# Kernel tuning notes

Hardware: AMD Instinct MI355X
Metric: run time of the kernel (lower is better)

Reference implementation:

```python
import jax, jax.numpy as jnp
import numpy as np

B, S, L = 4, 4096, 256

def _dense_init(key, fan_in, fan_out):
    lim = float(np.sqrt(6.0 / (fan_in + fan_out)))  # glorot_uniform (keras Dense default)
    return jax.random.uniform(key, (fan_in, fan_out), minval=-lim, maxval=lim, dtype=jnp.float32)

def setup_inputs() -> dict:
    key = jax.random.key(0)
    ks = jax.random.split(key, 12)
    causal = jnp.triu(jnp.ones((S, S), jnp.float32), k=1)  # 1 where future -> masked
    return {
        "tar_position": jax.random.uniform(ks[0], (B, S), dtype=jnp.float32),
        "current_pos": jax.random.uniform(ks[1], (B, S), dtype=jnp.float32),
        "tar_inp": jax.random.normal(ks[2], (B, S), dtype=jnp.float32),
        "training": 0,
        "pos_mask": jnp.zeros((B, S, S), jnp.float32),  # unused in call
        "tar_mask": jnp.broadcast_to(causal, (B, S, S)),
        "wq_w": _dense_init(ks[3], 2, L), "wq_b": jnp.zeros((L,), jnp.float32),
        "wk_w": _dense_init(ks[4], 2, L), "wk_b": jnp.zeros((L,), jnp.float32),
        "wv_w": _dense_init(ks[5], 1, L), "wv_b": jnp.zeros((L,), jnp.float32),
        "a2_w": _dense_init(ks[6], L, 128), "a2_b": jnp.zeros((128,), jnp.float32),
        "a3_w": _dense_init(ks[7], 1, 128), "a3_b": jnp.zeros((128,), jnp.float32),
        "a4_w": _dense_init(ks[8], 128, 32), "a4_b": jnp.zeros((32,), jnp.float32),
        "a5_w": _dense_init(ks[9], 32, 2), "a5_b": jnp.zeros((2,), jnp.float32),
    }

def reference(tar_position, current_pos, tar_inp, training, pos_mask, tar_mask,
              wq_w, wq_b, wk_w, wk_b, wv_w, wv_b,
              a2_w, a2_b, a3_w, a3_b, a4_w, a4_b, a5_w, a5_b):
    cp = current_pos[:, :, None]                         # [B,S,1]
    tar = jnp.stack([tar_position, tar_inp], axis=-1)    # [B,S,2]
    # matmul([B,S,l,1],[B,S,1,1]) == elementwise scale by current_pos
    q = (tar @ wq_w + wq_b) * cp                         # [B,S,L]
    k = (tar @ wk_w + wk_b) * cp                         # [B,S,L]
    v = tar_inp[:, :, None] * wv_w[0] + wv_b             # [B,S,L] (Dense fan_in=1)
    scale = 1.0 / jnp.sqrt(jnp.asarray(q.shape[-1], q.dtype))
    scores = jnp.einsum('bsl,btl->bst', q, k) * scale + tar_mask * (-1e9)
    attn = jax.nn.softmax(scores, axis=-1)               # [B,S,S]
    tar_attn = jnp.einsum('bst,btl->bsl', attn, v)       # [B,S,L]
    h = tar_attn @ a2_w + a2_b + cp * a3_w[0] + a3_b     # [B,S,128]
    h = jax.nn.leaky_relu(h, 0.2)                        # tf.nn.leaky_relu alpha=0.2
    h = jax.nn.leaky_relu(h @ a4_w + a4_b, 0.2)          # [B,S,32]
    out = h @ a5_w + a5_b                                # [B,S,2]
    return jnp.squeeze(out)
```

## Files before the change

### kernel.cpp

```cpp
#include <hip/hip_runtime.h>


#define SEQ 4096
#define NB 4


__global__ __launch_bounds__(256) void pre_kernel(
    const float* __restrict__ wq_w, const float* __restrict__ wq_b,
    const float* __restrict__ wk_w, const float* __restrict__ wk_b,
    const float* __restrict__ wv_w, const float* __restrict__ wv_b,
    const float* __restrict__ a2_w, const float* __restrict__ a2_b,
    const float* __restrict__ a3_w, const float* __restrict__ a3_b,
    float* __restrict__ ws)
{
    int tid = threadIdx.x;
    if (tid < 128) {
        float c1 = 0.f, c3 = 0.f;
        for (int l = 0; l < 256; ++l) {
            float a2 = a2_w[l * 128 + tid];
            c1 += wv_w[l] * a2;
            c3 += wv_b[l] * a2;
        }
        ws[16 + tid]  = c1;
        ws[160 + tid] = a3_w[tid];
        ws[288 + tid] = c3 + a2_b[tid] + a3_b[tid];
    } else if (tid < 128 + 9) {
        int idx = tid - 128;
        int i = idx / 3, j = idx % 3;
        const float* qv = (i == 0) ? wq_w : (i == 1) ? (wq_w + 256) : wq_b;
        const float* kv = (j == 0) ? wk_w : (j == 1) ? (wk_w + 256) : wk_b;
        float m = 0.f;
        for (int l = 0; l < 256; ++l) m += qv[l] * kv[l];
        ws[i * 3 + j] = m;
    }
}

__global__ __launch_bounds__(256) void attn_kernel(
    const float* __restrict__ tp,
    const float* __restrict__ cp,
    const float* __restrict__ ti,
    const float* __restrict__ ws,
    float* __restrict__ A)
{
    const int wave = (blockIdx.x * blockDim.x + threadIdx.x) >> 6;
    const int lane = threadIdx.x & 63;
    const int b = wave >> 11;
    const int r = wave & 2047;

    const float M00 = ws[0], M01 = ws[1], M02 = ws[2];
    const float M10 = ws[3], M11 = ws[4], M12 = ws[5];
    const float M20 = ws[6], M21 = ws[7], M22 = ws[8];
    const float scale = 0.0625f;

    const float* __restrict__ tpb = tp + b * SEQ;
    const float* __restrict__ cpb = cp + b * SEQ;
    const float* __restrict__ tib = ti + b * SEQ;

    #pragma unroll
    for (int pick = 0; pick < 2; ++pick) {
        const int s = pick ? (SEQ - 1 - r) : r;
        const float cps = cpb[s], tps = tpb[s], tis = tib[s];
        const float x0 = cps * tps, x1 = cps * tis, x2 = cps;
        const float d0 = scale * (M00 * x0 + M10 * x1 + M20 * x2);
        const float d1 = scale * (M01 * x0 + M11 * x1 + M21 * x2);
        const float d2 = scale * (M02 * x0 + M12 * x1 + M22 * x2);

        float lsum = 0.f, asum = 0.f;
        for (int t = lane; t <= s; t += 64) {
            const float cpt = cpb[t];
            const float tpt = tpb[t];
            const float tit = tib[t];
            const float sc = cpt * (d0 * tpt + d1 * tit + d2);
            const float w = __expf(sc);
            lsum += w;
            asum += w * tit;
        }
        #pragma unroll
        for (int off = 32; off; off >>= 1) {
            lsum += __shfl_down(lsum, off, 64);
            asum += __shfl_down(asum, off, 64);
        }
        if (lane == 0) A[b * SEQ + s] = asum / lsum;
    }
}

__global__ __launch_bounds__(64) void mlp_kernel(
    const float* __restrict__ A,
    const float* __restrict__ cp,
    const float* __restrict__ ws,
    const float* __restrict__ a4_w,
    const float* __restrict__ a4_b,
    const float* __restrict__ a5_w,
    const float* __restrict__ a5_b,
    float* __restrict__ out)
{
    __shared__ float sc1[128], sc2[128], sc3[128];
    __shared__ float sa4[128 * 32];
    const int tid = threadIdx.x;
    for (int i = tid; i < 128; i += 64) {
        sc1[i] = ws[16 + i];
        sc2[i] = ws[160 + i];
        sc3[i] = ws[288 + i];
    }
    for (int i = tid; i < 128 * 32; i += 64) sa4[i] = a4_w[i];
    __syncthreads();

    const int p = blockIdx.x * 64 + tid;
    const float Av = A[p], cpv = cp[p];

    float acc[32];
    #pragma unroll
    for (int j2 = 0; j2 < 32; ++j2) acc[j2] = a4_b[j2];

    for (int j = 0; j < 128; ++j) {
        float h = Av * sc1[j] + cpv * sc2[j] + sc3[j];
        h = (h >= 0.f) ? h : 0.2f * h;
        #pragma unroll
        for (int j2 = 0; j2 < 32; ++j2) acc[j2] += h * sa4[j * 32 + j2];
    }

    float o0 = a5_b[0], o1 = a5_b[1];
    #pragma unroll
    for (int j2 = 0; j2 < 32; ++j2) {
        const float h2 = (acc[j2] >= 0.f) ? acc[j2] : 0.2f * acc[j2];
        o0 += h2 * a5_w[j2 * 2 + 0];
        o1 += h2 * a5_w[j2 * 2 + 1];
    }
    out[p * 2 + 0] = o0;
    out[p * 2 + 1] = o1;
}

extern "C" void kernel_launch(void* const* d_in, const int* in_sizes, int n_in,
                              void* d_out, int out_size, void* d_ws, size_t ws_size,
                              hipStream_t stream) {
    const float* tp   = (const float*)d_in[0];
    const float* cp   = (const float*)d_in[1];
    const float* ti   = (const float*)d_in[2];
    const float* wq_w = (const float*)d_in[6];
    const float* wq_b = (const float*)d_in[7];
    const float* wk_w = (const float*)d_in[8];
    const float* wk_b = (const float*)d_in[9];
    const float* wv_w = (const float*)d_in[10];
    const float* wv_b = (const float*)d_in[11];
    const float* a2_w = (const float*)d_in[12];
    const float* a2_b = (const float*)d_in[13];
    const float* a3_w = (const float*)d_in[14];
    const float* a3_b = (const float*)d_in[15];
    const float* a4_w = (const float*)d_in[16];
    const float* a4_b = (const float*)d_in[17];
    const float* a5_w = (const float*)d_in[18];
    const float* a5_b = (const float*)d_in[19];

    float* ws  = (float*)d_ws;
    float* A   = ws + 512;
    float* out = (float*)d_out;

    hipLaunchKernelGGL(pre_kernel, dim3(1), dim3(256), 0, stream,
                       wq_w, wq_b, wk_w, wk_b, wv_w, wv_b,
                       a2_w, a2_b, a3_w, a3_b, ws);
    hipLaunchKernelGGL(attn_kernel, dim3(2048), dim3(256), 0, stream,
                       tp, cp, ti, ws, A);
    hipLaunchKernelGGL(mlp_kernel, dim3(256), dim3(64), 0, stream,
                       A, cp, ws, a4_w, a4_b, a5_w, a5_b, out);
}
```

Before: 475.2 us.

## Pack per-position features into float4 array and unroll attention loop by two

```diff
diff --git a/kernel.cpp b/kernel.cpp
--- a/kernel.cpp
+++ b/kernel.cpp
@@ -6,6 +6,8 @@
 
 
 __global__ __launch_bounds__(256) void pre_kernel(
+    const float* __restrict__ tp, const float* __restrict__ cp,
+    const float* __restrict__ ti,
     const float* __restrict__ wq_w, const float* __restrict__ wq_b,
     const float* __restrict__ wk_w, const float* __restrict__ wk_b,
     const float* __restrict__ wv_w, const float* __restrict__ wv_b,
@@ -13,32 +15,35 @@
     const float* __restrict__ a3_w, const float* __restrict__ a3_b,
     float* __restrict__ ws)
 {
-    int tid = threadIdx.x;
+    const int tid = threadIdx.x;
+    const int p = blockIdx.x * 256 + tid;
+    const float cpv = cp[p], tpv = tp[p], tiv = ti[p];
+    float4* X = (float4*)(ws + 1024);
+    X[p] = make_float4(cpv * tpv, cpv * tiv, cpv, tiv);
+
+    if (blockIdx.x != 0) return;
     if (tid < 128) {
         float c1 = 0.f, c3 = 0.f;
         for (int l = 0; l < 256; ++l) {
-            float a2 = a2_w[l * 128 + tid];
-            c1 += wv_w[l] * a2;
-            c3 += wv_b[l] * a2;
+            const float a2 = a2_w[l * 128 + tid];
+            c1 = fmaf(wv_w[l], a2, c1);
+            c3 = fmaf(wv_b[l], a2, c3);
         }
         ws[16 + tid]  = c1;
         ws[160 + tid] = a3_w[tid];
         ws[288 + tid] = c3 + a2_b[tid] + a3_b[tid];
-    } else if (tid < 128 + 9) {
-        int idx = tid - 128;
-        int i = idx / 3, j = idx % 3;
+    } else if (tid < 137) {
+        const int idx = tid - 128;
+        const int i = idx / 3, j = idx % 3;
         const float* qv = (i == 0) ? wq_w : (i == 1) ? (wq_w + 256) : wq_b;
         const float* kv = (j == 0) ? wk_w : (j == 1) ? (wk_w + 256) : wk_b;
         float m = 0.f;
-        for (int l = 0; l < 256; ++l) m += qv[l] * kv[l];
-        ws[i * 3 + j] = m;
+        for (int l = 0; l < 256; ++l) m = fmaf(qv[l], kv[l], m);
+        ws[i * 3 + j] = m * 0.0625f;
     }
 }
 
 __global__ __launch_bounds__(256) void attn_kernel(
-    const float* __restrict__ tp,
-    const float* __restrict__ cp,
-    const float* __restrict__ ti,
     const float* __restrict__ ws,
     float* __restrict__ A)
 {
@@ -50,30 +55,35 @@
     const float M00 = ws[0], M01 = ws[1], M02 = ws[2];
     const float M10 = ws[3], M11 = ws[4], M12 = ws[5];
     const float M20 = ws[6], M21 = ws[7], M22 = ws[8];
-    const float scale = 0.0625f;
 
-    const float* __restrict__ tpb = tp + b * SEQ;
-    const float* __restrict__ cpb = cp + b * SEQ;
-    const float* __restrict__ tib = ti + b * SEQ;
+    const float4* __restrict__ Xb = (const float4*)(ws + 1024) + b * SEQ;
 
     #pragma unroll
     for (int pick = 0; pick < 2; ++pick) {
         const int s = pick ? (SEQ - 1 - r) : r;
-        const float cps = cpb[s], tps = tpb[s], tis = tib[s];
-        const float x0 = cps * tps, x1 = cps * tis, x2 = cps;
-        const float d0 = scale * (M00 * x0 + M10 * x1 + M20 * x2);
-        const float d1 = scale * (M01 * x0 + M11 * x1 + M21 * x2);
-        const float d2 = scale * (M02 * x0 + M12 * x1 + M22 * x2);
+        const float4 xs = Xb[s];
+        const float d0 = M00 * xs.x + M10 * xs.y + M20 * xs.z;
+        const float d1 = M01 * xs.x + M11 * xs.y + M21 * xs.z;
+        const float d2 = M02 * xs.x + M12 * xs.y + M22 * xs.z;
 
         float lsum = 0.f, asum = 0.f;
-        for (int t = lane; t <= s; t += 64) {
-            const float cpt = cpb[t];
-            const float tpt = tpb[t];
-            const float tit = tib[t];
-            const float sc = cpt * (d0 * tpt + d1 * tit + d2);
-            const float w = __expf(sc);
-            lsum += w;
-            asum += w * tit;
+        int t = lane;
+        for (; t + 64 <= s; t += 128) {
+            const float4 xa = Xb[t];
+            const float4 xb = Xb[t + 64];
+            const float sa = fmaf(d0, xa.x, fmaf(d1, xa.y, d2 * xa.z));
+            const float sb = fmaf(d0, xb.x, fmaf(d1, xb.y, d2 * xb.z));
+            const float wa = __expf(sa);
+            const float wb = __expf(sb);
+            lsum += wa + wb;
+            asum = fmaf(wa, xa.w, fmaf(wb, xb.w, asum));
+        }
+        if (t <= s) {
+            const float4 xa = Xb[t];
+            const float sa = fmaf(d0, xa.x, fmaf(d1, xa.y, d2 * xa.z));
+            const float wa = __expf(sa);
+            lsum += wa;
+            asum = fmaf(wa, xa.w, asum);
         }
         #pragma unroll
         for (int off = 32; off; off >>= 1) {
@@ -95,39 +105,50 @@
     float* __restrict__ out)
 {
     __shared__ float sc1[128], sc2[128], sc3[128];
-    __shared__ float sa4[128 * 32];
+    __shared__ float4 sa4[1024];
     const int tid = threadIdx.x;
     for (int i = tid; i < 128; i += 64) {
         sc1[i] = ws[16 + i];
         sc2[i] = ws[160 + i];
         sc3[i] = ws[288 + i];
     }
-    for (int i = tid; i < 128 * 32; i += 64) sa4[i] = a4_w[i];
+    const float4* a4v = (const float4*)a4_w;
+    for (int i = tid; i < 1024; i += 64) sa4[i] = a4v[i];
     __syncthreads();
 
     const int p = blockIdx.x * 64 + tid;
     const float Av = A[p], cpv = cp[p];
 
-    float acc[32];
+    float4 acc[8];
     #pragma unroll
-    for (int j2 = 0; j2 < 32; ++j2) acc[j2] = a4_b[j2];
+    for (int k = 0; k < 8; ++k) acc[k] = ((const float4*)a4_b)[k];
 
     for (int j = 0; j < 128; ++j) {
-        float h = Av * sc1[j] + cpv * sc2[j] + sc3[j];
+        float h = fmaf(Av, sc1[j], fmaf(cpv, sc2[j], sc3[j]));
         h = (h >= 0.f) ? h : 0.2f * h;
         #pragma unroll
-        for (int j2 = 0; j2 < 32; ++j2) acc[j2] += h * sa4[j * 32 + j2];
+        for (int k = 0; k < 8; ++k) {
+            const float4 w4 = sa4[j * 8 + k];
+            acc[k].x = fmaf(h, w4.x, acc[k].x);
+            acc[k].y = fmaf(h, w4.y, acc[k].y);
+            acc[k].z = fmaf(h, w4.z, acc[k].z);
+            acc[k].w = fmaf(h, w4.w, acc[k].w);
+        }
     }
 
     float o0 = a5_b[0], o1 = a5_b[1];
     #pragma unroll
-    for (int j2 = 0; j2 < 32; ++j2) {
-        const float h2 = (acc[j2] >= 0.f) ? acc[j2] : 0.2f * acc[j2];
-        o0 += h2 * a5_w[j2 * 2 + 0];
-        o1 += h2 * a5_w[j2 * 2 + 1];
+    for (int k = 0; k < 8; ++k) {
+        const float* av = (const float*)&acc[k];
+        #pragma unroll
+        for (int c = 0; c < 4; ++c) {
+            const int j2 = k * 4 + c;
+            const float h2 = (av[c] >= 0.f) ? av[c] : 0.2f * av[c];
+            o0 = fmaf(h2, a5_w[j2 * 2 + 0], o0);
+            o1 = fmaf(h2, a5_w[j2 * 2 + 1], o1);
+        }
     }
-    out[p * 2 + 0] = o0;
-    out[p * 2 + 1] = o1;
+    ((float2*)out)[p] = make_float2(o0, o1);
 }
 
 extern "C" void kernel_launch(void* const* d_in, const int* in_sizes, int n_in,
@@ -152,14 +173,14 @@
     const float* a5_b = (const float*)d_in[19];
 
     float* ws  = (float*)d_ws;
-    float* A   = ws + 512;
+    float* A   = ws + 66560;
     float* out = (float*)d_out;
 
-    hipLaunchKernelGGL(pre_kernel, dim3(1), dim3(256), 0, stream,
-                       wq_w, wq_b, wk_w, wk_b, wv_w, wv_b,
+    hipLaunchKernelGGL(pre_kernel, dim3(64), dim3(256), 0, stream,
+                       tp, cp, ti, wq_w, wq_b, wk_w, wk_b, wv_w, wv_b,
                        a2_w, a2_b, a3_w, a3_b, ws);
     hipLaunchKernelGGL(attn_kernel, dim3(2048), dim3(256), 0, stream,
-                       tp, cp, ti, ws, A);
+                       ws, A);
     hipLaunchKernelGGL(mlp_kernel, dim3(256), dim3(64), 0, stream,
                        A, cp, ws, a4_w, a4_b, a5_w, a5_b, out);
 }
```

After: 483.1 us. Within noise of the previous version (+1.6%).
